# Optimization experiments

Hardware: AMD Instinct MI355X
Metric: run time of the kernel (lower is better)

## Reference

```python
import jax, jax.numpy as jnp
import numpy as np

LN_EPS = 1e-5

def layer_norm(x, g, b):
    mu = jnp.mean(x, axis=-1, keepdims=True)
    var = jnp.mean(jnp.square(x - mu), axis=-1, keepdims=True)
    return (x - mu) * jax.lax.rsqrt(var + LN_EPS) * g + b

def ternary_quant(w):
    # BitNet b1.58-style ternary quantization with straight-through estimator
    scale = 1.0 / jnp.clip(jnp.mean(jnp.abs(w)), 1e-5)
    wq = jnp.clip(jnp.round(w * scale), -1.0, 1.0) / scale
    return w + jax.lax.stop_gradient(wq - w)

def setup_inputs() -> dict:
    key = jax.random.key(0)
    ks = jax.random.split(key, 3)
    dim, hidden = 1024, 4096
    B, S = 8, 1024
    x = jax.random.normal(ks[0], (B, S, dim), dtype=jnp.float32)
    w1 = jax.random.normal(ks[1], (hidden, dim), dtype=jnp.float32) * 0.02
    w2 = jax.random.normal(ks[2], (dim, hidden), dtype=jnp.float32) * 0.02
    return {
        "x": x,
        "ln1_g": jnp.ones((dim,), jnp.float32), "ln1_b": jnp.zeros((dim,), jnp.float32),
        "w1": w1, "b1": jnp.zeros((hidden,), jnp.float32),
        "ln2_g": jnp.ones((hidden,), jnp.float32), "ln2_b": jnp.zeros((hidden,), jnp.float32),
        "w2": w2, "b2": jnp.zeros((dim,), jnp.float32),
    }

def reference(x, ln1_g, ln1_b, w1, b1, ln2_g, ln2_b, w2, b2):
    h = layer_norm(x, ln1_g, ln1_b)
    h = jnp.einsum('bsd,hd->bsh', h, ternary_quant(w1)) + b1  # [B,S,hidden]
    h = jax.nn.gelu(h, approximate=False)  # nn.GELU default is exact erf
    h = layer_norm(h, ln2_g, ln2_b)
    out = jnp.einsum('bsh,dh->bsd', h, ternary_quant(w2)) + b2  # [B,S,dim]
    return out
```

## Files before the change

### kernel.cpp

```cpp
#include <hip/hip_runtime.h>
#include <cstdint>
#include <cstddef>

#define DIM   1024
#define HID   4096
#define MROWS 8192

typedef __attribute__((ext_vector_type(8))) __bf16 bf16x8;
typedef __attribute__((ext_vector_type(4))) float  f32x4;
typedef __attribute__((ext_vector_type(4))) int    i32x4;

__device__ __forceinline__ unsigned short f2bf(float f) {
  unsigned int u = __float_as_uint(f);
  u += 0x7fffu + ((u >> 16) & 1u);
  return (unsigned short)(u >> 16);
}
__device__ __forceinline__ float bf2f(unsigned int lo16) {
  return __uint_as_float(lo16 << 16);
}

__device__ __forceinline__ float fast_gelu(float v) {
  float u = v * (0.79788456080286536f + 0.035677408136300125f * v * v);
  float e = __builtin_amdgcn_exp2f(u * 2.8853900817779268f);
  float r = __builtin_amdgcn_rcpf(e + 1.0f);
  return v - v * r;
}

__device__ __forceinline__ void gld16(const void* g, void* l) {
  auto* gp = reinterpret_cast<__attribute__((address_space(1))) unsigned int*>(
      reinterpret_cast<uintptr_t>(g));
  auto* lp = reinterpret_cast<__attribute__((address_space(3))) unsigned int*>(
      reinterpret_cast<uintptr_t>(l));
  __builtin_amdgcn_global_load_lds(gp, lp, 16, 0, 0);
}

__device__ __forceinline__ void wave_reduce2(float& a, float& b) {
#pragma unroll
  for (int off = 32; off > 0; off >>= 1) {
    a += __shfl_xor(a, off, 64);
    b += __shfl_xor(b, off, 64);
  }
}
__device__ __forceinline__ float wave_reduce_max(float m) {
#pragma unroll
  for (int off = 32; off > 0; off >>= 1) m = fmaxf(m, __shfl_xor(m, off, 64));
  return m;
}

__device__ __forceinline__ void block_reduce2(float& a, float& b, int tid) {
  __shared__ float red[8];
  __syncthreads();
  wave_reduce2(a, b);
  if ((tid & 63) == 0) { red[tid >> 6] = a; red[4 + (tid >> 6)] = b; }
  __syncthreads();
  a = red[0] + red[1] + red[2] + red[3];
  b = red[4] + red[5] + red[6] + red[7];
}

__global__ __launch_bounds__(256)
void prep_kernel(const float* __restrict__ w1, const float* __restrict__ w2,
                 float* __restrict__ part,
                 const float* __restrict__ x, const float* __restrict__ g,
                 const float* __restrict__ b, unsigned int* __restrict__ xn8,
                 float* __restrict__ invs) {
  int tid = threadIdx.x;
  int bid = blockIdx.x;
  if (bid < 2048) {
    const float* w = (bid < 1024) ? w1 : w2;
    int blk = bid & 1023;
    const float4* base = (const float4*)w + (size_t)blk * 1024;
    float s = 0.f;
#pragma unroll
    for (int i = 0; i < 4; ++i) {
      float4 v = base[tid + i * 256];
      s += fabsf(v.x) + fabsf(v.y) + fabsf(v.z) + fabsf(v.w);
    }
#pragma unroll
    for (int off = 32; off > 0; off >>= 1) s += __shfl_xor(s, off, 64);
    __shared__ float red[4];
    if ((tid & 63) == 0) red[tid >> 6] = s;
    __syncthreads();
    if (tid == 0) part[bid] = red[0] + red[1] + red[2] + red[3];
  } else {
    const int row  = (bid - 2048) * 4 + (tid >> 6);
    const int lane = tid & 63;
    const float4* xr = (const float4*)(x + (size_t)row * DIM);
    const float4* g4 = (const float4*)g;
    const float4* b4 = (const float4*)b;
    float4 v[4];
    float s = 0.f, ss = 0.f;
#pragma unroll
    for (int p = 0; p < 4; ++p) {
      v[p] = xr[lane + 64 * p];
      s  += v[p].x + v[p].y + v[p].z + v[p].w;
      ss += v[p].x * v[p].x + v[p].y * v[p].y + v[p].z * v[p].z + v[p].w * v[p].w;
    }
    wave_reduce2(s, ss);
    float mu  = s * (1.0f / DIM);
    float var = ss * (1.0f / DIM) - mu * mu;
    float rs  = rsqrtf(var + 1e-5f);
    float n[4][4];
    float amax = 0.f;
#pragma unroll
    for (int p = 0; p < 4; ++p) {
      float4 gg = g4[lane + 64 * p];
      float4 bb = b4[lane + 64 * p];
      n[p][0] = (v[p].x - mu) * rs * gg.x + bb.x;
      n[p][1] = (v[p].y - mu) * rs * gg.y + bb.y;
      n[p][2] = (v[p].z - mu) * rs * gg.z + bb.z;
      n[p][3] = (v[p].w - mu) * rs * gg.w + bb.w;
#pragma unroll
      for (int c = 0; c < 4; ++c) amax = fmaxf(amax, fabsf(n[p][c]));
    }
    amax = wave_reduce_max(amax);
    float sc, iv;
    if (amax < 1e-20f) { sc = 0.f; iv = 0.f; }
    else               { sc = 127.0f / amax; iv = amax * (1.0f / 127.0f); }
    if (lane == 0) invs[row] = iv;
    unsigned int* dst = xn8 + (size_t)row * 256;
#pragma unroll
    for (int p = 0; p < 4; ++p) {
      unsigned r = 0;
#pragma unroll
      for (int c = 0; c < 4; ++c) {
        int q = (int)rintf(n[p][c] * sc);
        r |= ((unsigned)q & 0xffu) << (8 * c);
      }
      dst[lane + 64 * p] = r;
    }
  }
}

__global__ __launch_bounds__(256)
void quant_kernel(const float* __restrict__ part,
                  const float* __restrict__ w1, unsigned int* __restrict__ q1,
                  const float* __restrict__ w2, unsigned short* __restrict__ q2,
                  const float* __restrict__ g2, const float* __restrict__ b2,
                  const float* __restrict__ bias2,
                  float* __restrict__ Sg, float* __restrict__ Cb,
                  float* __restrict__ scal) {
  int bid = blockIdx.x, tid = threadIdx.x;
  const int lane = tid & 63;
  const float4* psrc = (const float4*)(part + ((bid < 512) ? 0 : 1024));
  float a = 0.f, dummy = 0.f;
#pragma unroll
  for (int p = 0; p < 4; ++p) {
    float4 pv = psrc[lane + 64 * p];
    a += pv.x + pv.y + pv.z + pv.w;
  }
  wave_reduce2(a, dummy);
  float mean = fmaxf(a * (1.0f / 4194304.0f), 1e-5f);
  float sc = 1.0f / mean;

  if (bid < 512) {
    if (bid == 0 && tid == 0) scal[0] = mean;
    const int n4 = 1048576;
    int i = bid * 256 + tid;
    for (; i < n4; i += 512 * 256) {
      float4 v = ((const float4*)w1)[i];
      int t0 = (int)fminf(fmaxf(rintf(v.x * sc), -1.f), 1.f);
      int t1 = (int)fminf(fmaxf(rintf(v.y * sc), -1.f), 1.f);
      int t2 = (int)fminf(fmaxf(rintf(v.z * sc), -1.f), 1.f);
      int t3 = (int)fminf(fmaxf(rintf(v.w * sc), -1.f), 1.f);
      unsigned r = ((unsigned)t0 & 0xffu) | (((unsigned)t1 & 0xffu) << 8) |
                   (((unsigned)t2 & 0xffu) << 16) | (((unsigned)t3 & 0xffu) << 24);
      q1[i] = r;
    }
  } else {
    const int d = bid - 512;
    if (d == 0 && tid == 0) scal[1] = mean;
    const float4* wr = (const float4*)(w2 + (size_t)d * HID);
    const float4* g4 = (const float4*)g2;
    const float4* b4 = (const float4*)b2;
    uint2* qr = (uint2*)(q2 + (size_t)d * HID);
    float s1 = 0.f, s2 = 0.f;
#pragma unroll
    for (int i = 0; i < 4; ++i) {
      int idx = tid + 256 * i;
      float4 wv = wr[idx], gv = g4[idx], bv = b4[idx];
      float t0 = fminf(fmaxf(rintf(wv.x * sc), -1.f), 1.f);
      float t1 = fminf(fmaxf(rintf(wv.y * sc), -1.f), 1.f);
      float t2 = fminf(fmaxf(rintf(wv.z * sc), -1.f), 1.f);
      float t3 = fminf(fmaxf(rintf(wv.w * sc), -1.f), 1.f);
      s1 += gv.x * t0 + gv.y * t1 + gv.z * t2 + gv.w * t3;
      s2 += bv.x * t0 + bv.y * t1 + bv.z * t2 + bv.w * t3;
      uint2 r;
      r.x = (unsigned)f2bf(t0 * gv.x) | ((unsigned)f2bf(t1 * gv.y) << 16);
      r.y = (unsigned)f2bf(t2 * gv.z) | ((unsigned)f2bf(t3 * gv.w) << 16);
      qr[idx] = r;
    }
    block_reduce2(s1, s2, tid);
    if (tid == 0) {
      Sg[d] = mean * s1;
      Cb[d] = mean * s2 + bias2[d];
    }
  }
}

__global__ __launch_bounds__(256)
void gemm1_i8(const unsigned char* __restrict__ A,
              const unsigned char* __restrict__ B,
              unsigned short* __restrict__ H,
              const float* __restrict__ wscale_ptr,
              const float* __restrict__ invs,
              const float* __restrict__ bias,
              float2* __restrict__ sbuf2) {
  __shared__ unsigned char sA[2][128 * 64];
  __shared__ unsigned char sB[2][128 * 64];

  const int tid  = threadIdx.x;
  const int lane = tid & 63;
  const int wave = tid >> 6;
  const int wm   = wave & 1;
  const int wn   = wave >> 1;

  const int nbx  = gridDim.x;
  const int id   = blockIdx.y * nbx + blockIdx.x;
  const int xcd  = id & 7;
  const int slot = id >> 3;
  const int bandsPerXcd = gridDim.y >> 3;
  const int band = xcd * bandsPerXcd + slot / nbx;
  const int col  = slot - (slot / nbx) * nbx;
  const int bm   = band * 128;
  const int bn   = col * 128;

  const int csw = ((tid & 3) ^ ((tid >> 3) & 3)) * 16;
  const unsigned char* Ab = A + (size_t)(bm + (tid >> 2)) * 1024 + csw;
  const unsigned char* Bb = B + (size_t)(bn + (tid >> 2)) * 1024 + csw;

  i32x4 acc[4][4] = {};

  const int rowA = (wm * 64 + (lane & 15)) * 64;
  const int rowB = (wn * 64 + (lane & 15)) * 64;
  const int kc = (((lane >> 4) ^ ((lane >> 1) & 3))) * 16;

  gld16(Ab,             (char*)&sA[0][0] + tid * 16);
  gld16(Ab + 64 * 1024, (char*)&sA[0][0] + 4096 + tid * 16);
  gld16(Bb,             (char*)&sB[0][0] + tid * 16);
  gld16(Bb + 64 * 1024, (char*)&sB[0][0] + 4096 + tid * 16);
  asm volatile("s_waitcnt vmcnt(0)" ::: "memory");
  __builtin_amdgcn_s_barrier();

  for (int t = 0; t < 16; ++t) {
    const int cur = t & 1;
    const size_t kn = (t + 1 < 16) ? (size_t)(t + 1) * 64 : 0;
    gld16(Ab + kn,             (char*)&sA[cur ^ 1][0] + tid * 16);
    gld16(Ab + 64 * 1024 + kn, (char*)&sA[cur ^ 1][0] + 4096 + tid * 16);
    gld16(Bb + kn,             (char*)&sB[cur ^ 1][0] + tid * 16);
    gld16(Bb + 64 * 1024 + kn, (char*)&sB[cur ^ 1][0] + 4096 + tid * 16);
    const unsigned char* a = &sA[cur][0];
    const unsigned char* b = &sB[cur][0];
    i32x4 af[4], bfr[4];
#pragma unroll
    for (int i = 0; i < 4; ++i) af[i]  = *(const i32x4*)(a + rowA + i * 1024 + kc);
#pragma unroll
    for (int j = 0; j < 4; ++j) bfr[j] = *(const i32x4*)(b + rowB + j * 1024 + kc);
    __builtin_amdgcn_s_setprio(1);
#pragma unroll
    for (int i = 0; i < 4; ++i)
#pragma unroll
      for (int j = 0; j < 4; ++j)
        acc[i][j] = __builtin_amdgcn_mfma_i32_16x16x64_i8(af[i], bfr[j], acc[i][j], 0, 0, 0);
    __builtin_amdgcn_s_setprio(0);
    asm volatile("s_waitcnt vmcnt(0)" ::: "memory");
    __builtin_amdgcn_s_barrier();
  }

  const float wscale = *wscale_ptr;
  float bv[4];
#pragma unroll
  for (int j = 0; j < 4; ++j) bv[j] = bias[bn + wn * 64 + j * 16 + (lane & 15)];
#pragma unroll
  for (int i = 0; i < 4; ++i) {
    const int m0 = bm + wm * 64 + i * 16 + ((lane >> 4) << 2);
    float asc[4];
#pragma unroll
    for (int r = 0; r < 4; ++r) asc[r] = wscale * invs[m0 + r];
#pragma unroll
    for (int r = 0; r < 4; ++r) {
      float s = 0.f, ss = 0.f;
#pragma unroll
      for (int j = 0; j < 4; ++j) {
        const int n = bn + wn * 64 + j * 16 + (lane & 15);
        float v = fast_gelu((float)acc[i][j][r] * asc[r] + bv[j]);
        H[(size_t)(m0 + r) * HID + n] = f2bf(v);
        s += v; ss += v * v;
      }
#pragma unroll
      for (int off = 1; off < 16; off <<= 1) {
        s  += __shfl_xor(s, off, 64);
        ss += __shfl_xor(ss, off, 64);
      }
      if ((lane & 15) == 0) {
        sbuf2[((size_t)(m0 + r) << 6) + (col << 1) + wn] = make_float2(s, ss);
      }
    }
  }
}

__global__ __launch_bounds__(256)
void murs_fin(const float2* __restrict__ sbuf2, const float* __restrict__ meanp,
              float2* __restrict__ murs) {
  const int row  = blockIdx.x * 4 + (threadIdx.x >> 6);
  const int lane = threadIdx.x & 63;
  float2 v = sbuf2[((size_t)row << 6) + lane];
  float s = v.x, ss = v.y;
  wave_reduce2(s, ss);
  if (lane == 0) {
    float mu  = s * (1.0f / HID);
    float var = ss * (1.0f / HID) - mu * mu;
    float rs  = rsqrtf(var + 1e-5f);
    murs[row] = make_float2(rs * meanp[1], -rs * mu);
  }
}

__global__ __launch_bounds__(512, 2)
void gemm2_v3(const unsigned short* __restrict__ A,
              const unsigned short* __restrict__ B,
              float* __restrict__ C,
              const float2* __restrict__ murs,
              const float* __restrict__ Sg,
              const float* __restrict__ Cb) {
  __shared__ unsigned short sA[2][256 * 64];
  __shared__ unsigned short sB[2][128 * 64];

  const int tid  = threadIdx.x;
  const int lane = tid & 63;
  const int wave = tid >> 6;
  const int wm   = wave >> 1;
  const int wn   = wave & 1;

  const int id   = blockIdx.y * 8 + blockIdx.x;
  const int xcd  = id & 7;
  const int slot = id >> 3;
  const int band = xcd * 4 + (slot >> 3);
  const int col  = slot & 7;
  const int bm   = band * 256;
  const int bn   = col * 128;

  const int csw = ((tid & 7) ^ ((tid >> 3) & 7)) << 3;
  const unsigned short* Ab = A + (size_t)(bm + (tid >> 3)) * 4096 + csw;
  const unsigned short* Bb = B + (size_t)(bn + (tid >> 3)) * 4096 + csw;

  const int rowAb = (wm * 64 + (lane & 15)) * 128;
  const int rowBb = (wn * 64 + (lane & 15)) * 128;
  const int hi    = lane >> 4;
  const int ck0   = ((hi)     ^ (lane & 7)) << 4;
  const int ck1   = ((hi + 4) ^ (lane & 7)) << 4;

  f32x4 acc[4][4] = {};

#pragma unroll
  for (int i = 0; i < 4; ++i) gld16(Ab + (size_t)i * 262144, (char*)&sA[0][0] + i * 8192 + tid * 16);
#pragma unroll
  for (int i = 0; i < 2; ++i) gld16(Bb + (size_t)i * 262144, (char*)&sB[0][0] + i * 8192 + tid * 16);
  asm volatile("s_waitcnt vmcnt(0)" ::: "memory");
  __builtin_amdgcn_s_barrier();

  for (int t = 0; t < 64; ++t) {
    const int cur = t & 1;
    const size_t kn = (t + 1 < 64) ? (size_t)(t + 1) * 64 : 0;
#pragma unroll
    for (int i = 0; i < 4; ++i)
      gld16(Ab + (size_t)i * 262144 + kn, (char*)&sA[cur ^ 1][0] + i * 8192 + tid * 16);
#pragma unroll
    for (int i = 0; i < 2; ++i)
      gld16(Bb + (size_t)i * 262144 + kn, (char*)&sB[cur ^ 1][0] + i * 8192 + tid * 16);
    const char* a = (const char*)&sA[cur][0];
    const char* b = (const char*)&sB[cur][0];
    bf16x8 af[4][2], bfr[4][2];
#pragma unroll
    for (int i = 0; i < 4; ++i) {
      af[i][0] = *(const bf16x8*)(a + rowAb + i * 2048 + ck0);
      af[i][1] = *(const bf16x8*)(a + rowAb + i * 2048 + ck1);
    }
#pragma unroll
    for (int j = 0; j < 4; ++j) {
      bfr[j][0] = *(const bf16x8*)(b + rowBb + j * 2048 + ck0);
      bfr[j][1] = *(const bf16x8*)(b + rowBb + j * 2048 + ck1);
    }
    __builtin_amdgcn_s_setprio(1);
#pragma unroll
    for (int i = 0; i < 4; ++i)
#pragma unroll
      for (int j = 0; j < 4; ++j)
        acc[i][j] = __builtin_amdgcn_mfma_f32_16x16x32_bf16(af[i][0], bfr[j][0], acc[i][j], 0, 0, 0);
#pragma unroll
    for (int i = 0; i < 4; ++i)
#pragma unroll
      for (int j = 0; j < 4; ++j)
        acc[i][j] = __builtin_amdgcn_mfma_f32_16x16x32_bf16(af[i][1], bfr[j][1], acc[i][j], 0, 0, 0);
    __builtin_amdgcn_s_setprio(0);
    asm volatile("s_waitcnt vmcnt(0)" ::: "memory");
    __builtin_amdgcn_s_barrier();
  }

  float sg[4], cb[4];
#pragma unroll
  for (int j = 0; j < 4; ++j) {
    const int n = bn + wn * 64 + j * 16 + (lane & 15);
    sg[j] = Sg[n];
    cb[j] = Cb[n];
  }
#pragma unroll
  for (int i = 0; i < 4; ++i) {
    const int m0 = bm + wm * 64 + i * 16 + (hi << 2);
#pragma unroll
    for (int r = 0; r < 4; ++r) {
      float2 ab = murs[m0 + r];
#pragma unroll
      for (int j = 0; j < 4; ++j) {
        const int n = bn + wn * 64 + j * 16 + (lane & 15);
        C[(size_t)(m0 + r) * 1024 + n] = ab.x * acc[i][j][r] + ab.y * sg[j] + cb[j];
      }
    }
  }
}

extern "C" void kernel_launch(void* const* d_in, const int* in_sizes, int n_in,
                              void* d_out, int out_size, void* d_ws, size_t ws_size,
                              hipStream_t stream) {
  const float* x     = (const float*)d_in[0];
  const float* g1    = (const float*)d_in[1];
  const float* b1v   = (const float*)d_in[2];
  const float* w1    = (const float*)d_in[3];
  const float* bias1 = (const float*)d_in[4];
  const float* g2    = (const float*)d_in[5];
  const float* b2v   = (const float*)d_in[6];
  const float* w2    = (const float*)d_in[7];
  const float* bias2 = (const float*)d_in[8];
  float* out = (float*)d_out;

  char* ws = (char*)d_ws;
  float* scal          = (float*)ws;
  float* part          = (float*)(ws + 64);
  float* invs          = (float*)(ws + 16384);
  unsigned int* q1     = (unsigned int*)(ws + 65536);
  unsigned short* q2   = (unsigned short*)(ws + 65536 + 4194304);
  unsigned int* xn8    = (unsigned int*)((char*)q2 + 8388608);
  unsigned short* h    = (unsigned short*)((char*)xn8 + 8388608);
  float2* murs         = (float2*)((char*)h + 67108864);
  float* Sg            = (float*)(murs + 8192);
  float* Cb            = Sg + 1024;
  float2* sbuf2        = (float2*)(Cb + 1024);

  prep_kernel<<<4096, 256, 0, stream>>>(w1, w2, part, x, g1, b1v, xn8, invs);
  quant_kernel<<<1536, 256, 0, stream>>>(part, w1, q1, w2, q2, g2, b2v, bias2, Sg, Cb, scal);
  gemm1_i8<<<dim3(HID / 128, MROWS / 128), 256, 0, stream>>>(
      (const unsigned char*)xn8, (const unsigned char*)q1, h, scal + 0, invs, bias1, sbuf2);
  murs_fin<<<MROWS / 4, 256, 0, stream>>>(sbuf2, scal, murs);
  gemm2_v3<<<dim3(8, 32), 512, 0, stream>>>(h, q2, out, murs, Sg, Cb);
}
```

Baseline: 245.4 us.

## Split K across wave pairs in gemm2 with LDS reduction epilogue

Reorganizes gemm2's eight waves into two K-halves, with each wave computing a 128x64 output tile over half of each K slice. B fragments loaded from LDS are reused across twice as many MFMAs, reducing LDS read traffic per MFMA. Partial sums from the second K-half are reduced through shared memory in two rounds before the fused LayerNorm/bias epilogue. This doubles per-wave accumulator registers, which risks spilling under the 512x2 launch bound, and adds barriers to the epilogue.

Result: slower. 252.3 us (+2.8%).

```diff
diff --git a/kernel.cpp b/kernel.cpp
--- a/kernel.cpp
+++ b/kernel.cpp
@@ -315,7 +315,7 @@
 }
 
 __global__ __launch_bounds__(512, 2)
-void gemm2_v3(const unsigned short* __restrict__ A,
+void gemm2_v4(const unsigned short* __restrict__ A,
               const unsigned short* __restrict__ B,
               float* __restrict__ C,
               const float2* __restrict__ murs,
@@ -327,8 +327,9 @@
   const int tid  = threadIdx.x;
   const int lane = tid & 63;
   const int wave = tid >> 6;
-  const int wm   = wave >> 1;
   const int wn   = wave & 1;
+  const int wm   = (wave >> 1) & 1;
+  const int wk   = wave >> 2;
 
   const int id   = blockIdx.y * 8 + blockIdx.x;
   const int xcd  = id & 7;
@@ -342,13 +343,12 @@
   const unsigned short* Ab = A + (size_t)(bm + (tid >> 3)) * 4096 + csw;
   const unsigned short* Bb = B + (size_t)(bn + (tid >> 3)) * 4096 + csw;
 
-  const int rowAb = (wm * 64 + (lane & 15)) * 128;
-  const int rowBb = (wn * 64 + (lane & 15)) * 128;
+  const int rowAb = (wm * 128 + (lane & 15)) * 128;
+  const int rowBb = (wn * 64  + (lane & 15)) * 128;
   const int hi    = lane >> 4;
-  const int ck0   = ((hi)     ^ (lane & 7)) << 4;
-  const int ck1   = ((hi + 4) ^ (lane & 7)) << 4;
-
-  f32x4 acc[4][4] = {};
+  const int ck    = ((wk * 4 + hi) ^ (lane & 7)) << 4;
+
+  f32x4 acc[8][4] = {};
 
 #pragma unroll
   for (int i = 0; i < 4; ++i) gld16(Ab + (size_t)i * 262144, (char*)&sA[0][0] + i * 8192 + tid * 16);
@@ -368,29 +368,24 @@
       gld16(Bb + (size_t)i * 262144 + kn, (char*)&sB[cur ^ 1][0] + i * 8192 + tid * 16);
     const char* a = (const char*)&sA[cur][0];
     const char* b = (const char*)&sB[cur][0];
-    bf16x8 af[4][2], bfr[4][2];
-#pragma unroll
-    for (int i = 0; i < 4; ++i) {
-      af[i][0] = *(const bf16x8*)(a + rowAb + i * 2048 + ck0);
-      af[i][1] = *(const bf16x8*)(a + rowAb + i * 2048 + ck1);
-    }
-#pragma unroll
-    for (int j = 0; j < 4; ++j) {
-      bfr[j][0] = *(const bf16x8*)(b + rowBb + j * 2048 + ck0);
-      bfr[j][1] = *(const bf16x8*)(b + rowBb + j * 2048 + ck1);
-    }
-    __builtin_amdgcn_s_setprio(1);
-#pragma unroll
-    for (int i = 0; i < 4; ++i)
-#pragma unroll
-      for (int j = 0; j < 4; ++j)
-        acc[i][j] = __builtin_amdgcn_mfma_f32_16x16x32_bf16(af[i][0], bfr[j][0], acc[i][j], 0, 0, 0);
-#pragma unroll
-    for (int i = 0; i < 4; ++i)
-#pragma unroll
-      for (int j = 0; j < 4; ++j)
-        acc[i][j] = __builtin_amdgcn_mfma_f32_16x16x32_bf16(af[i][1], bfr[j][1], acc[i][j], 0, 0, 0);
-    __builtin_amdgcn_s_setprio(0);
+    bf16x8 bfr[4];
+#pragma unroll
+    for (int j = 0; j < 4; ++j) bfr[j] = *(const bf16x8*)(b + rowBb + j * 2048 + ck);
+#pragma unroll
+    for (int h2 = 0; h2 < 2; ++h2) {
+      bf16x8 af[4];
+#pragma unroll
+      for (int i = 0; i < 4; ++i)
+        af[i] = *(const bf16x8*)(a + rowAb + (h2 * 4 + i) * 2048 + ck);
+      __builtin_amdgcn_s_setprio(1);
+#pragma unroll
+      for (int i = 0; i < 4; ++i)
+#pragma unroll
+        for (int j = 0; j < 4; ++j)
+          acc[h2 * 4 + i][j] =
+              __builtin_amdgcn_mfma_f32_16x16x32_bf16(af[i], bfr[j], acc[h2 * 4 + i][j], 0, 0, 0);
+      __builtin_amdgcn_s_setprio(0);
+    }
     asm volatile("s_waitcnt vmcnt(0)" ::: "memory");
     __builtin_amdgcn_s_barrier();
   }
@@ -402,16 +397,33 @@
     sg[j] = Sg[n];
     cb[j] = Cb[n];
   }
-#pragma unroll
-  for (int i = 0; i < 4; ++i) {
-    const int m0 = bm + wm * 64 + i * 16 + (hi << 2);
-#pragma unroll
-    for (int r = 0; r < 4; ++r) {
-      float2 ab = murs[m0 + r];
-#pragma unroll
-      for (int j = 0; j < 4; ++j) {
-        const int n = bn + wn * 64 + j * 16 + (lane & 15);
-        C[(size_t)(m0 + r) * 1024 + n] = ab.x * acc[i][j][r] + ab.y * sg[j] + cb[j];
+  float* red = (float*)&sA[0][0];
+  for (int round = 0; round < 2; ++round) {
+    __builtin_amdgcn_s_barrier();
+    if (wk == 1 && wm == round) {
+#pragma unroll
+      for (int i = 0; i < 8; ++i)
+#pragma unroll
+        for (int j = 0; j < 4; ++j)
+          *(f32x4*)(red + wn * 8192 + (i * 4 + j) * 256 + lane * 4) = acc[i][j];
+    }
+    __builtin_amdgcn_s_barrier();
+    if (wk == 0 && wm == round) {
+#pragma unroll
+      for (int i = 0; i < 8; ++i) {
+        const int m0 = bm + wm * 128 + i * 16 + (hi << 2);
+#pragma unroll
+        for (int j = 0; j < 4; ++j)
+          acc[i][j] += *(const f32x4*)(red + wn * 8192 + (i * 4 + j) * 256 + lane * 4);
+#pragma unroll
+        for (int r = 0; r < 4; ++r) {
+          float2 ab = murs[m0 + r];
+#pragma unroll
+          for (int j = 0; j < 4; ++j) {
+            const int n = bn + wn * 64 + j * 16 + (lane & 15);
+            C[(size_t)(m0 + r) * 1024 + n] = ab.x * acc[i][j][r] + ab.y * sg[j] + cb[j];
+          }
+        }
       }
     }
   }
@@ -449,5 +461,5 @@
   gemm1_i8<<<dim3(HID / 128, MROWS / 128), 256, 0, stream>>>(
       (const unsigned char*)xn8, (const unsigned char*)q1, h, scal + 0, invs, bias1, sbuf2);
   murs_fin<<<MROWS / 4, 256, 0, stream>>>(sbuf2, scal, murs);
-  gemm2_v3<<<dim3(8, 32), 512, 0, stream>>>(h, q2, out, murs, Sg, Cb);
-}
+  gemm2_v4<<<dim3(8, 32), 512, 0, stream>>>(h, q2, out, murs, Sg, Cb);
+}
```
